# Performance work log

Hardware: AMD Instinct MI355X
Metric: run time of the kernel (lower is better)

Reference implementation:

```python
import jax, jax.numpy as jnp
import numpy as np

N_HEAD = 16
KEY_DIM = 1024
D_HEAD = KEY_DIM // N_HEAD
THRESHOLD = 0.1
EPS = 1e-7


def xavier_uniform(key, out_dim, in_dim):
    limit = np.sqrt(6.0 / (in_dim + out_dim)).astype(np.float32)
    return jax.random.uniform(key, (out_dim, in_dim), jnp.float32, -limit, limit)


def setup_inputs() -> dict:
    key = jax.random.key(0)
    k1, k2, k3, k4, k5 = jax.random.split(key, 5)
    B, Sq, Skv = 4, 1024, 1024
    q = jax.random.normal(k1, (B, Sq, 1024), jnp.float32)
    k = jax.random.normal(k2, (B, Skv, KEY_DIM), jnp.float32)
    v = jax.random.normal(k3, (B, Skv, 1024), jnp.float32)
    Wq = xavier_uniform(k4, KEY_DIM, 1024)  # nn.Linear weight (out, in)
    Wk = xavier_uniform(k5, KEY_DIM, KEY_DIM)
    k_mask = jnp.ones((B, Skv), jnp.int32)
    return {"q": q, "k": k, "v": v, "Wq": Wq, "Wk": Wk, "k_mask": k_mask}


def cum_thresholded_softmax(logits, threshold=THRESHOLD):
    # softmax, then zero out the smallest entries whose cumulative mass < threshold,
    # renormalize, with straight-through gradient to the plain softmax.
    s = jax.nn.softmax(logits, axis=-1)
    order = jnp.argsort(s, axis=-1)                      # ascending, like torch.sort(descending=False)
    s_sorted = jnp.take_along_axis(s, order, axis=-1)
    csum = jnp.cumsum(s_sorted, axis=-1)
    mask_sorted = 1.0 - (csum < threshold).astype(s.dtype)
    inv = jnp.argsort(order, axis=-1)                    # inverse permutation == scatter back
    mask = jnp.take_along_axis(mask_sorted, inv, axis=-1)
    act = mask * s
    norm = act / (jnp.sum(act, axis=-1, keepdims=True) + EPS)
    return jax.lax.stop_gradient(norm - s) + s


def reference(q, k, v, Wq, Wk, k_mask):
    B, Sq, _ = q.shape
    Skv = k.shape[1]
    qp = jnp.einsum('bsd,ed->bse', q, Wq)  # (B,Sq,key_dim)
    kp = jnp.einsum('bsd,ed->bse', k, Wk)  # (B,Skv,key_dim)
    qh = qp.reshape(B, Sq, N_HEAD, D_HEAD).transpose(0, 2, 1, 3)   # (B,H,Sq,Dh)
    kh = kp.reshape(B, Skv, N_HEAD, D_HEAD).transpose(0, 2, 1, 3)  # (B,H,Skv,Dh)
    scale = jnp.asarray(1.0 / np.sqrt(D_HEAD), qh.dtype)
    scores = jnp.einsum('bhqd,bhkd->bhqk', qh, kh) * scale         # (B,H,Sq,Skv)
    neg = jnp.asarray(jnp.finfo(scores.dtype).min, scores.dtype)
    scores = jnp.where(k_mask[:, None, None, :] > 0, scores, neg)
    attn = cum_thresholded_softmax(scores)                         # (B,H,Sq,Skv)
    attn = attn.mean(axis=1)                                       # average heads -> (B,Sq,Skv)
    out = jnp.einsum('bqk,bkd->bqd', attn, v)                      # (B,Sq,value_dim)
    return out, attn
```

## Files before the change

kernel.cpp:

```cpp
#include <hip/hip_runtime.h>

typedef unsigned short u16;
typedef unsigned int u32;
typedef __attribute__((ext_vector_type(8))) short bf16x8;
typedef __attribute__((ext_vector_type(4))) float f32x4;

#define MFMA __builtin_amdgcn_mfma_f32_16x16x32_bf16

__device__ __forceinline__ u16 f2bf(float x) {
    union { float f; u32 u; } a; a.f = x;
    return (u16)((a.u + 0x7fffu + ((a.u >> 16) & 1u)) >> 16);
}
__device__ __forceinline__ float bf2f(u16 h) {
    union { u32 u; float f; } a; a.u = ((u32)h) << 16;
    return a.f;
}

__device__ __forceinline__ void cvt_store(char* Lh, char* Ll, int row, int c4, float4 x) {
    u16 h0 = f2bf(x.x), h1 = f2bf(x.y), h2 = f2bf(x.z), h3 = f2bf(x.w);
    u16 l0 = f2bf(x.x - bf2f(h0)), l1 = f2bf(x.y - bf2f(h1));
    u16 l2 = f2bf(x.z - bf2f(h2)), l3 = f2bf(x.w - bf2f(h3));
    const int byte = row * 128 + ((((c4 >> 1) << 4) ^ ((row & 7) << 4)) | ((c4 & 1) << 3));
    *(uint2*)&Lh[byte] = make_uint2((u32)h0 | ((u32)h1 << 16), (u32)h2 | ((u32)h3 << 16));
    *(uint2*)&Ll[byte] = make_uint2((u32)l0 | ((u32)l1 << 16), (u32)l2 | ((u32)l3 << 16));
}

__device__ __forceinline__ bf16x8 ldfrag(const char* L, int row, int kk, int lg) {
    const int cb = (kk * 64 + (lg << 4)) ^ ((row & 7) << 4);
    return *(const bf16x8*)&L[row * 128 + cb];
}

template<int MODE>
__global__ __launch_bounds__(256, 3)
void gemmT(const float* __restrict__ A, const float* __restrict__ B,
           void* __restrict__ C0, void* __restrict__ C1)
{
    __shared__ __align__(16) char Ah[8192], Al[8192], Bh[16384], Bl[16384];
    const int tid = threadIdx.x;
    const int m0 = blockIdx.y * 64;
    const int n0 = blockIdx.x * 128;
    const int w = tid >> 6, l = tid & 63;
    const int wr = (w >> 1) * 32, wc = (w & 1) * 64;
    const int lm = l & 15, lg = l >> 4;
    const float* Bp = B + (MODE == 2 ? ((size_t)(m0 >> 10) << 20) : (size_t)0);

    f32x4 acc[2][4];
#pragma unroll
    for (int a = 0; a < 2; ++a)
#pragma unroll
        for (int bq = 0; bq < 4; ++bq) acc[a][bq] = (f32x4){0.f, 0.f, 0.f, 0.f};

    const int ar = tid >> 2, ac = tid & 3;
    const int br = tid >> 1, bc = tid & 1;

    for (int k0 = 0; k0 < 1024; k0 += 64) {
        __syncthreads();
        const float* As = &A[(size_t)(m0 + ar) * 1024 + k0 + ac * 16];
#pragma unroll
        for (int j = 0; j < 4; ++j) cvt_store(Ah, Al, ar, ac * 4 + j, *(const float4*)&As[j * 4]);
        const float* Bs = &Bp[(size_t)(n0 + br) * 1024 + k0 + bc * 32];
#pragma unroll
        for (int j = 0; j < 8; ++j) cvt_store(Bh, Bl, br, bc * 8 + j, *(const float4*)&Bs[j * 4]);
        __syncthreads();
#pragma unroll
        for (int kk = 0; kk < 2; ++kk) {
            bf16x8 aH[2], aL[2], bH[4], bL[4];
#pragma unroll
            for (int mi = 0; mi < 2; ++mi) {
                aH[mi] = ldfrag(Ah, wr + mi * 16 + lm, kk, lg);
                aL[mi] = ldfrag(Al, wr + mi * 16 + lm, kk, lg);
            }
#pragma unroll
            for (int ni = 0; ni < 4; ++ni) {
                bH[ni] = ldfrag(Bh, wc + ni * 16 + lm, kk, lg);
                bL[ni] = ldfrag(Bl, wc + ni * 16 + lm, kk, lg);
            }
#pragma unroll
            for (int mi = 0; mi < 2; ++mi)
#pragma unroll
                for (int ni = 0; ni < 4; ++ni) {
                    acc[mi][ni] = MFMA(aH[mi], bH[ni], acc[mi][ni], 0, 0, 0);
                    acc[mi][ni] = MFMA(aH[mi], bL[ni], acc[mi][ni], 0, 0, 0);
                    acc[mi][ni] = MFMA(aL[mi], bH[ni], acc[mi][ni], 0, 0, 0);
                }
        }
    }

#pragma unroll
    for (int mi = 0; mi < 2; ++mi)
#pragma unroll
        for (int ni = 0; ni < 4; ++ni) {
            const int m = m0 + wr + mi * 16 + lg * 4;
            const int n = n0 + wc + ni * 16 + lm;
            if (MODE == 0) {
                const int bb = n >> 10, s = n & 1023;
                const int h = m >> 6, dh = m & 63;
                const size_t base = (((size_t)(bb * 16 + h) << 10) + s) * 64 + dh;
                u16 hh[4], ll[4];
#pragma unroll
                for (int i = 0; i < 4; ++i) {
                    hh[i] = f2bf(acc[mi][ni][i]);
                    ll[i] = f2bf(acc[mi][ni][i] - bf2f(hh[i]));
                }
                *(uint2*)&((u16*)C0)[base] = make_uint2((u32)hh[0] | ((u32)hh[1] << 16),
                                                        (u32)hh[2] | ((u32)hh[3] << 16));
                *(uint2*)&((u16*)C1)[base] = make_uint2((u32)ll[0] | ((u32)ll[1] << 16),
                                                        (u32)ll[2] | ((u32)ll[3] << 16));
            } else {
#pragma unroll
                for (int i = 0; i < 4; ++i)
                    ((float*)C0)[(size_t)(m + i) * 1024 + n] = acc[mi][ni][i];
            }
        }
}

__global__ __launch_bounds__(512, 4)
void attn2_k(const u16* __restrict__ qhh, const u16* __restrict__ qhl,
             const u16* __restrict__ khh, const u16* __restrict__ khl,
             const int* __restrict__ kmask, float* __restrict__ attn)
{
    __shared__ __align__(16) float S[16][1028];
    __shared__ __align__(16) float mneg[1024];
    const int tid = threadIdx.x;
    const int b = blockIdx.x >> 7;
    const int q0 = ((blockIdx.x >> 1) & 63) << 4;
    const int p = blockIdx.x & 1;
    const int w = tid >> 6, l = tid & 63;
    const int lm = l & 15, lg = l >> 4;

    for (int i = tid; i < 1024; i += 512)
        mneg[i] = (kmask[(b << 10) + i] > 0) ? 0.f : -3.0e38f;

    float racc0[16], racc1[16];
#pragma unroll
    for (int j = 0; j < 16; ++j) { racc0[j] = 0.f; racc1[j] = 0.f; }

    for (int t = 0; t < 8; ++t) {
        const int h = (t << 1) | p;
        const size_t hb = (size_t)((b << 4) + h) << 10;
        const size_t qoff = (hb + q0 + lm) * 64 + (lg << 3);
        const bf16x8 bh0 = *(const bf16x8*)&qhh[qoff];
        const bf16x8 bh1 = *(const bf16x8*)&qhh[qoff + 32];
        const bf16x8 bl0 = *(const bf16x8*)&qhl[qoff];
        const bf16x8 bl1 = *(const bf16x8*)&qhl[qoff + 32];

        f32x4 acc[8];
#pragma unroll
        for (int mi = 0; mi < 8; ++mi) acc[mi] = (f32x4){0.f, 0.f, 0.f, 0.f};

        const int kvb = w << 7;
#pragma unroll
        for (int mi = 0; mi < 8; ++mi) {
            const size_t aoff = (hb + kvb + (mi << 4) + lm) * 64 + (lg << 3);
            const bf16x8 ah0 = *(const bf16x8*)&khh[aoff];
            const bf16x8 ah1 = *(const bf16x8*)&khh[aoff + 32];
            const bf16x8 al0 = *(const bf16x8*)&khl[aoff];
            const bf16x8 al1 = *(const bf16x8*)&khl[aoff + 32];
            acc[mi] = MFMA(ah0, bh0, acc[mi], 0, 0, 0);
            acc[mi] = MFMA(ah0, bl0, acc[mi], 0, 0, 0);
            acc[mi] = MFMA(al0, bh0, acc[mi], 0, 0, 0);
            acc[mi] = MFMA(ah1, bh1, acc[mi], 0, 0, 0);
            acc[mi] = MFMA(ah1, bl1, acc[mi], 0, 0, 0);
            acc[mi] = MFMA(al1, bh1, acc[mi], 0, 0, 0);
        }
        __syncthreads();
#pragma unroll
        for (int mi = 0; mi < 8; ++mi)
            *(f32x4*)&S[lm][kvb + (mi << 4) + (lg << 2)] = acc[mi];
        __syncthreads();

        float sa[16], sb[16];
#pragma unroll
        for (int jj = 0; jj < 4; ++jj) {
            const f32x4 va = *(const f32x4*)&S[2 * w][jj * 256 + l * 4];
            const f32x4 vb = *(const f32x4*)&S[2 * w + 1][jj * 256 + l * 4];
            const f32x4 vm = *(const f32x4*)&mneg[jj * 256 + l * 4];
#pragma unroll
            for (int ii = 0; ii < 4; ++ii) {
                sa[jj * 4 + ii] = va[ii] * 0.125f + vm[ii];
                sb[jj * 4 + ii] = vb[ii] * 0.125f + vm[ii];
            }
        }
        float ma = -3.0e38f, mb = -3.0e38f;
#pragma unroll
        for (int j = 0; j < 16; ++j) { ma = fmaxf(ma, sa[j]); mb = fmaxf(mb, sb[j]); }
#pragma unroll
        for (int off = 32; off; off >>= 1) { ma = fmaxf(ma, __shfl_xor(ma, off)); mb = fmaxf(mb, __shfl_xor(mb, off)); }
        float Za = 0.f, Zb = 0.f;
#pragma unroll
        for (int j = 0; j < 16; ++j) {
            sa[j] = __expf(sa[j] - ma); Za += sa[j];
            sb[j] = __expf(sb[j] - mb); Zb += sb[j];
        }
#pragma unroll
        for (int off = 32; off; off >>= 1) { Za += __shfl_xor(Za, off); Zb += __shfl_xor(Zb, off); }

        const float tga = 0.1f * Za, tgb = 0.1f * Zb;
        float loa = 0.f, hia = 1.f, lob = 0.f, hib = 1.f;
        for (int it = 0; it < 15; ++it) {
            const float ca = 0.5f * (loa + hia), cb = 0.5f * (lob + hib);
            float ta = 0.f, tb = 0.f;
#pragma unroll
            for (int j = 0; j < 16; ++j) {
                ta += (sa[j] <= ca) ? sa[j] : 0.f;
                tb += (sb[j] <= cb) ? sb[j] : 0.f;
            }
#pragma unroll
            for (int off = 32; off; off >>= 1) { ta += __shfl_xor(ta, off); tb += __shfl_xor(tb, off); }
            if (ta < tga) loa = ca; else hia = ca;
            if (tb < tgb) lob = cb; else hib = cb;
        }
        float Aa = 0.f, Ab = 0.f;
#pragma unroll
        for (int j = 0; j < 16; ++j) {
            Aa += (sa[j] > loa) ? sa[j] : 0.f;
            Ab += (sb[j] > lob) ? sb[j] : 0.f;
        }
#pragma unroll
        for (int off = 32; off; off >>= 1) { Aa += __shfl_xor(Aa, off); Ab += __shfl_xor(Ab, off); }
        const float rna = 1.f / (Aa + 1e-7f * Za);
        const float rnb = 1.f / (Ab + 1e-7f * Zb);
#pragma unroll
        for (int j = 0; j < 16; ++j) {
            racc0[j] += ((sa[j] > loa) ? sa[j] : 0.f) * rna;
            racc1[j] += ((sb[j] > lob) ? sb[j] : 0.f) * rnb;
        }
    }

#pragma unroll
    for (int jj = 0; jj < 4; ++jj)
#pragma unroll
        for (int ii = 0; ii < 4; ++ii) {
            atomicAdd(&attn[((size_t)(b << 10) + q0 + 2 * w) * 1024 + jj * 256 + l * 4 + ii],
                      racc0[jj * 4 + ii] * 0.0625f);
            atomicAdd(&attn[((size_t)(b << 10) + q0 + 2 * w + 1) * 1024 + jj * 256 + l * 4 + ii],
                      racc1[jj * 4 + ii] * 0.0625f);
        }
}

__global__ __launch_bounds__(256)
void vtT_k(const float* __restrict__ v, float* __restrict__ vt)
{
    __shared__ float T[64][65];
    const int b = blockIdx.z;
    const int kv0 = blockIdx.y << 6, d0 = blockIdx.x << 6;
    const int t = threadIdx.x;
    const int tr = t >> 4, tc = t & 15;
#pragma unroll
    for (int i = 0; i < 4; ++i) {
        const float4 x = *(const float4*)&v[(((size_t)b << 10) + kv0 + tr + i * 16) * 1024 + d0 + tc * 4];
        float* d = &T[tr + i * 16][tc * 4];
        d[0] = x.x; d[1] = x.y; d[2] = x.z; d[3] = x.w;
    }
    __syncthreads();
#pragma unroll
    for (int i = 0; i < 4; ++i) {
        const int dr = tr + i * 16;
        float4 o;
        o.x = T[tc * 4 + 0][dr]; o.y = T[tc * 4 + 1][dr];
        o.z = T[tc * 4 + 2][dr]; o.w = T[tc * 4 + 3][dr];
        *(float4*)&vt[(((size_t)b << 10) + d0 + dr) * 1024 + kv0 + tc * 4] = o;
    }
}

extern "C" void kernel_launch(void* const* d_in, const int* in_sizes, int n_in,
                              void* d_out, int out_size, void* d_ws, size_t ws_size,
                              hipStream_t stream) {
    const float* q  = (const float*)d_in[0];
    const float* k  = (const float*)d_in[1];
    const float* v  = (const float*)d_in[2];
    const float* Wq = (const float*)d_in[3];
    const float* Wk = (const float*)d_in[4];
    const int* kmask = (const int*)d_in[5];

    u16* qhh = (u16*)d_out;
    u16* qhl = qhh + 4194304;
    u16* khh = (u16*)d_ws;
    u16* khl = khh + 4194304;
    float* attn = (float*)d_out + 4194304;
    float* vt   = (float*)d_ws;
    float* out  = (float*)d_out;

    hipMemsetAsync(attn, 0, (size_t)4 * 1024 * 1024 * sizeof(float), stream);
    gemmT<0><<<dim3(32, 16), 256, 0, stream>>>(Wq, q, qhh, qhl);
    gemmT<0><<<dim3(32, 16), 256, 0, stream>>>(Wk, k, khh, khl);
    attn2_k<<<dim3(512), dim3(512), 0, stream>>>(qhh, qhl, khh, khl, kmask, attn);
    vtT_k<<<dim3(16, 16, 4), 256, 0, stream>>>(v, vt);
    gemmT<2><<<dim3(8, 64), 256, 0, stream>>>(attn, vt, out, nullptr);
}
```

Before: 530.5 us.

## Use DPP wave reductions, register-prefetch GEMM tiles, and cheaper bf16 split conversion

Wave-wide max/sum reductions in the thresholded-softmax loop switch from shfl_xor butterflies to DPP row shifts plus readlane. Per-lane partial sums are split into four independent accumulators to shorten dependency chains. The GEMM now prefetches the next K tile into registers while MFMAs run, and its bf16 hi/lo split uses perm instructions instead of separate shifts. The GEMM launch bound is lowered to 2 blocks per SM, giving it more registers for the prefetch buffers at the cost of occupancy.

Result: faster. 481.0 us (-9.3%).

```diff
diff --git a/kernel.cpp b/kernel.cpp
--- a/kernel.cpp
+++ b/kernel.cpp
@@ -16,13 +16,52 @@
     return a.f;
 }
 
+#define DPP_ADD(v, ctrl, rmask)                                                             \
+    v += __uint_as_float((u32)__builtin_amdgcn_update_dpp(0, (int)__float_as_uint(v),       \
+                                                          ctrl, rmask, 0xF, true))
+#define DPP_MAX(v, ctrl, rmask)                                                             \
+    v = fmaxf(v, __uint_as_float((u32)__builtin_amdgcn_update_dpp(                          \
+            (int)__float_as_uint(v), (int)__float_as_uint(v), ctrl, rmask, 0xF, false)))
+
+__device__ __forceinline__ float wsum(float v) {
+    DPP_ADD(v, 0x111, 0xF);
+    DPP_ADD(v, 0x112, 0xF);
+    DPP_ADD(v, 0x114, 0xF);
+    DPP_ADD(v, 0x118, 0xF);
+    DPP_ADD(v, 0x142, 0xA);
+    DPP_ADD(v, 0x143, 0xC);
+    return __uint_as_float((u32)__builtin_amdgcn_readlane((int)__float_as_uint(v), 63));
+}
+__device__ __forceinline__ float wmax(float v) {
+    DPP_MAX(v, 0x111, 0xF);
+    DPP_MAX(v, 0x112, 0xF);
+    DPP_MAX(v, 0x114, 0xF);
+    DPP_MAX(v, 0x118, 0xF);
+    DPP_MAX(v, 0x142, 0xA);
+    DPP_MAX(v, 0x143, 0xC);
+    return __uint_as_float((u32)__builtin_amdgcn_readlane((int)__float_as_uint(v), 63));
+}
+
 __device__ __forceinline__ void cvt_store(char* Lh, char* Ll, int row, int c4, float4 x) {
-    u16 h0 = f2bf(x.x), h1 = f2bf(x.y), h2 = f2bf(x.z), h3 = f2bf(x.w);
-    u16 l0 = f2bf(x.x - bf2f(h0)), l1 = f2bf(x.y - bf2f(h1));
-    u16 l2 = f2bf(x.z - bf2f(h2)), l3 = f2bf(x.w - bf2f(h3));
+    u32 ux = __float_as_uint(x.x), uy = __float_as_uint(x.y),
+        uz = __float_as_uint(x.z), uw = __float_as_uint(x.w);
+    u32 rx = ux + 0x7fffu + ((ux >> 16) & 1u), ry = uy + 0x7fffu + ((uy >> 16) & 1u);
+    u32 rz = uz + 0x7fffu + ((uz >> 16) & 1u), rw = uw + 0x7fffu + ((uw >> 16) & 1u);
+    u32 h01 = __builtin_amdgcn_perm(ry, rx, 0x07060302);
+    u32 h23 = __builtin_amdgcn_perm(rw, rz, 0x07060302);
+    float lx = x.x - __uint_as_float(rx & 0xffff0000u);
+    float ly = x.y - __uint_as_float(ry & 0xffff0000u);
+    float lz = x.z - __uint_as_float(rz & 0xffff0000u);
+    float lw = x.w - __uint_as_float(rw & 0xffff0000u);
+    u32 sx = __float_as_uint(lx); sx += 0x7fffu + ((sx >> 16) & 1u);
+    u32 sy = __float_as_uint(ly); sy += 0x7fffu + ((sy >> 16) & 1u);
+    u32 sz = __float_as_uint(lz); sz += 0x7fffu + ((sz >> 16) & 1u);
+    u32 sw = __float_as_uint(lw); sw += 0x7fffu + ((sw >> 16) & 1u);
+    u32 l01 = __builtin_amdgcn_perm(sy, sx, 0x07060302);
+    u32 l23 = __builtin_amdgcn_perm(sw, sz, 0x07060302);
     const int byte = row * 128 + ((((c4 >> 1) << 4) ^ ((row & 7) << 4)) | ((c4 & 1) << 3));
-    *(uint2*)&Lh[byte] = make_uint2((u32)h0 | ((u32)h1 << 16), (u32)h2 | ((u32)h3 << 16));
-    *(uint2*)&Ll[byte] = make_uint2((u32)l0 | ((u32)l1 << 16), (u32)l2 | ((u32)l3 << 16));
+    *(uint2*)&Lh[byte] = make_uint2(h01, h23);
+    *(uint2*)&Ll[byte] = make_uint2(l01, l23);
 }
 
 __device__ __forceinline__ bf16x8 ldfrag(const char* L, int row, int kk, int lg) {
@@ -31,7 +70,7 @@
 }
 
 template<int MODE>
-__global__ __launch_bounds__(256, 3)
+__global__ __launch_bounds__(256, 2)
 void gemmT(const float* __restrict__ A, const float* __restrict__ B,
            void* __restrict__ C0, void* __restrict__ C1)
 {
@@ -52,16 +91,28 @@
 
     const int ar = tid >> 2, ac = tid & 3;
     const int br = tid >> 1, bc = tid & 1;
+    const float* Aptr = &A[(size_t)(m0 + ar) * 1024 + ac * 16];
+    const float* Bptr = &Bp[(size_t)(n0 + br) * 1024 + bc * 32];
+
+    float4 pa[4], pb[8];
+#pragma unroll
+    for (int j = 0; j < 4; ++j) pa[j] = *(const float4*)&Aptr[j * 4];
+#pragma unroll
+    for (int j = 0; j < 8; ++j) pb[j] = *(const float4*)&Bptr[j * 4];
 
     for (int k0 = 0; k0 < 1024; k0 += 64) {
         __syncthreads();
-        const float* As = &A[(size_t)(m0 + ar) * 1024 + k0 + ac * 16];
-#pragma unroll
-        for (int j = 0; j < 4; ++j) cvt_store(Ah, Al, ar, ac * 4 + j, *(const float4*)&As[j * 4]);
-        const float* Bs = &Bp[(size_t)(n0 + br) * 1024 + k0 + bc * 32];
-#pragma unroll
-        for (int j = 0; j < 8; ++j) cvt_store(Bh, Bl, br, bc * 8 + j, *(const float4*)&Bs[j * 4]);
+#pragma unroll
+        for (int j = 0; j < 4; ++j) cvt_store(Ah, Al, ar, ac * 4 + j, pa[j]);
+#pragma unroll
+        for (int j = 0; j < 8; ++j) cvt_store(Bh, Bl, br, bc * 8 + j, pb[j]);
         __syncthreads();
+        if (k0 + 64 < 1024) {
+#pragma unroll
+            for (int j = 0; j < 4; ++j) pa[j] = *(const float4*)&Aptr[k0 + 64 + j * 4];
+#pragma unroll
+            for (int j = 0; j < 8; ++j) pb[j] = *(const float4*)&Bptr[k0 + 64 + j * 4];
+        }
 #pragma unroll
         for (int kk = 0; kk < 2; ++kk) {
             bf16x8 aH[2], aL[2], bH[4], bL[4];
@@ -181,43 +232,62 @@
                 sb[jj * 4 + ii] = vb[ii] * 0.125f + vm[ii];
             }
         }
-        float ma = -3.0e38f, mb = -3.0e38f;
-#pragma unroll
-        for (int j = 0; j < 16; ++j) { ma = fmaxf(ma, sa[j]); mb = fmaxf(mb, sb[j]); }
-#pragma unroll
-        for (int off = 32; off; off >>= 1) { ma = fmaxf(ma, __shfl_xor(ma, off)); mb = fmaxf(mb, __shfl_xor(mb, off)); }
-        float Za = 0.f, Zb = 0.f;
-#pragma unroll
-        for (int j = 0; j < 16; ++j) {
-            sa[j] = __expf(sa[j] - ma); Za += sa[j];
-            sb[j] = __expf(sb[j] - mb); Zb += sb[j];
-        }
-#pragma unroll
-        for (int off = 32; off; off >>= 1) { Za += __shfl_xor(Za, off); Zb += __shfl_xor(Zb, off); }
+        float ma = sa[0], mb = sb[0];
+#pragma unroll
+        for (int j = 1; j < 16; ++j) { ma = fmaxf(ma, sa[j]); mb = fmaxf(mb, sb[j]); }
+        ma = wmax(ma); mb = wmax(mb);
+
+        float z0 = 0.f, z1 = 0.f, z2 = 0.f, z3 = 0.f, y0 = 0.f, y1 = 0.f, y2 = 0.f, y3 = 0.f;
+#pragma unroll
+        for (int j = 0; j < 4; ++j) {
+            sa[j]      = __expf(sa[j]      - ma); z0 += sa[j];
+            sa[j + 4]  = __expf(sa[j + 4]  - ma); z1 += sa[j + 4];
+            sa[j + 8]  = __expf(sa[j + 8]  - ma); z2 += sa[j + 8];
+            sa[j + 12] = __expf(sa[j + 12] - ma); z3 += sa[j + 12];
+            sb[j]      = __expf(sb[j]      - mb); y0 += sb[j];
+            sb[j + 4]  = __expf(sb[j + 4]  - mb); y1 += sb[j + 4];
+            sb[j + 8]  = __expf(sb[j + 8]  - mb); y2 += sb[j + 8];
+            sb[j + 12] = __expf(sb[j + 12] - mb); y3 += sb[j + 12];
+        }
+        const float Za = wsum((z0 + z1) + (z2 + z3));
+        const float Zb = wsum((y0 + y1) + (y2 + y3));
 
         const float tga = 0.1f * Za, tgb = 0.1f * Zb;
         float loa = 0.f, hia = 1.f, lob = 0.f, hib = 1.f;
         for (int it = 0; it < 15; ++it) {
             const float ca = 0.5f * (loa + hia), cb = 0.5f * (lob + hib);
-            float ta = 0.f, tb = 0.f;
-#pragma unroll
-            for (int j = 0; j < 16; ++j) {
-                ta += (sa[j] <= ca) ? sa[j] : 0.f;
-                tb += (sb[j] <= cb) ? sb[j] : 0.f;
-            }
-#pragma unroll
-            for (int off = 32; off; off >>= 1) { ta += __shfl_xor(ta, off); tb += __shfl_xor(tb, off); }
+            float t0 = 0.f, t1 = 0.f, t2 = 0.f, t3 = 0.f;
+            float u0 = 0.f, u1 = 0.f, u2 = 0.f, u3 = 0.f;
+#pragma unroll
+            for (int j = 0; j < 4; ++j) {
+                t0 += (sa[j]      <= ca) ? sa[j]      : 0.f;
+                t1 += (sa[j + 4]  <= ca) ? sa[j + 4]  : 0.f;
+                t2 += (sa[j + 8]  <= ca) ? sa[j + 8]  : 0.f;
+                t3 += (sa[j + 12] <= ca) ? sa[j + 12] : 0.f;
+                u0 += (sb[j]      <= cb) ? sb[j]      : 0.f;
+                u1 += (sb[j + 4]  <= cb) ? sb[j + 4]  : 0.f;
+                u2 += (sb[j + 8]  <= cb) ? sb[j + 8]  : 0.f;
+                u3 += (sb[j + 12] <= cb) ? sb[j + 12] : 0.f;
+            }
+            const float ta = wsum((t0 + t1) + (t2 + t3));
+            const float tb = wsum((u0 + u1) + (u2 + u3));
             if (ta < tga) loa = ca; else hia = ca;
             if (tb < tgb) lob = cb; else hib = cb;
         }
-        float Aa = 0.f, Ab = 0.f;
-#pragma unroll
-        for (int j = 0; j < 16; ++j) {
-            Aa += (sa[j] > loa) ? sa[j] : 0.f;
-            Ab += (sb[j] > lob) ? sb[j] : 0.f;
-        }
-#pragma unroll
-        for (int off = 32; off; off >>= 1) { Aa += __shfl_xor(Aa, off); Ab += __shfl_xor(Ab, off); }
+        float a0 = 0.f, a1 = 0.f, a2 = 0.f, a3 = 0.f, b0 = 0.f, b1 = 0.f, b2 = 0.f, b3 = 0.f;
+#pragma unroll
+        for (int j = 0; j < 4; ++j) {
+            a0 += (sa[j]      > loa) ? sa[j]      : 0.f;
+            a1 += (sa[j + 4]  > loa) ? sa[j + 4]  : 0.f;
+            a2 += (sa[j + 8]  > loa) ? sa[j + 8]  : 0.f;
+            a3 += (sa[j + 12] > loa) ? sa[j + 12] : 0.f;
+            b0 += (sb[j]      > lob) ? sb[j]      : 0.f;
+            b1 += (sb[j + 4]  > lob) ? sb[j + 4]  : 0.f;
+            b2 += (sb[j + 8]  > lob) ? sb[j + 8]  : 0.f;
+            b3 += (sb[j + 12] > lob) ? sb[j + 12] : 0.f;
+        }
+        const float Aa = wsum((a0 + a1) + (a2 + a3));
+        const float Ab = wsum((b0 + b1) + (b2 + b3));
         const float rna = 1.f / (Aa + 1e-7f * Za);
         const float rnb = 1.f / (Ab + 1e-7f * Zb);
 #pragma unroll
```
